# Kernel tuning notes

Measured on AMD Instinct MI355X. Metric: run time of the kernel, lower is better.

Reference implementation:

```python
import jax, jax.numpy as jnp
import numpy as np

EPS = 1e-5

def activation_quant(x):
    # per-token absmax int8 quant-dequant (BitNet b1.58)
    scale = 127.0 / jnp.clip(jnp.max(jnp.abs(x), axis=-1, keepdims=True), EPS)
    q = jnp.clip(jnp.round(x * scale), -128.0, 127.0) / scale
    return q

def weight_quant(w):
    # per-tensor ternary quant-dequant: scale by 1/mean|w|, round, clamp to {-1,0,1}
    scale = 1.0 / jnp.clip(jnp.mean(jnp.abs(w)), EPS)
    q = jnp.clip(jnp.round(w * scale), -1.0, 1.0) / scale
    return q

def bitlinear(x, w):
    # x: [b, s, in], w: [out, in] (nn.Linear layout)
    return jnp.einsum('bsi,oi->bso', activation_quant(x), weight_quant(w))

def setup_inputs() -> dict:
    key = jax.random.key(0)
    k1, k2, k3, k4 = jax.random.split(key, 4)
    B, S, H, I = 2, 2048, 4096, 11008
    x = jax.random.normal(k1, (B, S, H), dtype=jnp.float32)
    w_gate = jax.random.normal(k2, (I, H), dtype=jnp.float32) * (1.0 / np.sqrt(H))
    w_up = jax.random.normal(k3, (I, H), dtype=jnp.float32) * (1.0 / np.sqrt(H))
    w_down = jax.random.normal(k4, (H, I), dtype=jnp.float32) * (1.0 / np.sqrt(I))
    return {"x": x, "w_gate": w_gate, "w_up": w_up, "w_down": w_down}

def reference(x, w_gate, w_up, w_down):
    g = bitlinear(x, w_gate)           # [B, S, I]
    u = bitlinear(x, w_up)             # [B, S, I]
    h = jnp.square(jax.nn.relu(g)) * u  # ReLU^2 gating
    return bitlinear(h, w_down)        # [B, S, H]
```

## Files before the change

kernel.cpp:

```cpp
#include <hip/hip_runtime.h>
#include <stdint.h>

#define TOKENS 4096
#define HDIM   4096
#define IDIM   11008
#define WELEMS 45088768L

using i32x4 = __attribute__((ext_vector_type(4))) int;
using s8x16 = __attribute__((ext_vector_type(16))) signed char;

__device__ __forceinline__ void async_load16(const void* g, void* l) {
  __builtin_amdgcn_global_load_lds(
      (const __attribute__((address_space(1))) void*)g,
      (__attribute__((address_space(3))) void*)l, 16, 0, 0);
}

__global__ __launch_bounds__(256) void wsum_kernel(
    const float* __restrict__ w0, const float* __restrict__ w1,
    const float* __restrict__ w2, double* __restrict__ dsum) {
  const float* w = (blockIdx.y == 0) ? w0 : (blockIdx.y == 1) ? w1 : w2;
  const long n4 = WELEMS / 4;
  long i = (long)blockIdx.x * blockDim.x + threadIdx.x;
  const long stride = (long)gridDim.x * blockDim.x;
  double s = 0.0;
  for (; i < n4; i += stride) {
    float4 v = ((const float4*)w)[i];
    s += (double)fabsf(v.x); s += (double)fabsf(v.y);
    s += (double)fabsf(v.z); s += (double)fabsf(v.w);
  }
  __shared__ double red[256];
  red[threadIdx.x] = s;
  __syncthreads();
  for (int off = 128; off; off >>= 1) {
    if (threadIdx.x < (unsigned)off) red[threadIdx.x] += red[threadIdx.x + off];
    __syncthreads();
  }
  if (threadIdx.x == 0) atomicAdd(&dsum[blockIdx.y], red[0]);
}

__global__ void wscale_kernel(const double* __restrict__ dsum, double* __restrict__ wsc) {
  int i = threadIdx.x;
  if (i < 3) {
    double mean = dsum[i] / (double)WELEMS;
    wsc[i] = 1.0 / fmax(mean, 1e-5);
  }
}

__global__ __launch_bounds__(256) void wquant_kernel(
    const float* __restrict__ w0, const float* __restrict__ w1, const float* __restrict__ w2,
    int8_t* __restrict__ q0, int8_t* __restrict__ q1, int8_t* __restrict__ q2,
    const double* __restrict__ wsc) {
  const int wi = blockIdx.y;
  const float* w = (wi == 0) ? w0 : (wi == 1) ? w1 : w2;
  int8_t* q = (wi == 0) ? q0 : (wi == 1) ? q1 : q2;
  const double sc = wsc[wi];
  long c = (long)blockIdx.x * blockDim.x + threadIdx.x;
  if (c * 16 >= WELEMS) return;
  const float4* src = (const float4*)(w + c * 16);
  s8x16 outv;
  #pragma unroll
  for (int j = 0; j < 4; ++j) {
    float4 v = src[j];
    double t0 = rint((double)v.x * sc); t0 = fmin(fmax(t0, -1.0), 1.0);
    double t1 = rint((double)v.y * sc); t1 = fmin(fmax(t1, -1.0), 1.0);
    double t2 = rint((double)v.z * sc); t2 = fmin(fmax(t2, -1.0), 1.0);
    double t3 = rint((double)v.w * sc); t3 = fmin(fmax(t3, -1.0), 1.0);
    outv[j*4+0] = (signed char)(int)t0; outv[j*4+1] = (signed char)(int)t1;
    outv[j*4+2] = (signed char)(int)t2; outv[j*4+3] = (signed char)(int)t3;
  }
  *(s8x16*)(q + c * 16) = outv;
}

__global__ __launch_bounds__(256) void xquant_kernel(
    const float* __restrict__ x, int8_t* __restrict__ xq, double* __restrict__ sx) {
  const int row = blockIdx.x;
  const float* xr = x + (long)row * HDIM;
  const float4* xr4 = (const float4*)xr;
  float m = 0.f;
  for (int i = threadIdx.x; i < HDIM / 4; i += 256) {
    float4 v = xr4[i];
    m = fmaxf(m, fmaxf(fmaxf(fabsf(v.x), fabsf(v.y)), fmaxf(fabsf(v.z), fabsf(v.w))));
  }
  __shared__ float red[256];
  red[threadIdx.x] = m;
  __syncthreads();
  for (int off = 128; off; off >>= 1) {
    if (threadIdx.x < (unsigned)off) red[threadIdx.x] = fmaxf(red[threadIdx.x], red[threadIdx.x + off]);
    __syncthreads();
  }
  __shared__ double s_sc;
  if (threadIdx.x == 0) {
    double sc = 127.0 / fmax((double)red[0], 1e-5);
    sx[row] = sc;
    s_sc = sc;
  }
  __syncthreads();
  const double sc = s_sc;
  s8x16 outv;
  #pragma unroll
  for (int j = 0; j < 4; ++j) {
    float4 v = xr4[threadIdx.x * 4 + j];
    double t0 = rint((double)v.x * sc); t0 = fmin(fmax(t0, -128.0), 127.0);
    double t1 = rint((double)v.y * sc); t1 = fmin(fmax(t1, -128.0), 127.0);
    double t2 = rint((double)v.z * sc); t2 = fmin(fmax(t2, -128.0), 127.0);
    double t3 = rint((double)v.w * sc); t3 = fmin(fmax(t3, -128.0), 127.0);
    outv[j*4+0] = (signed char)(int)t0; outv[j*4+1] = (signed char)(int)t1;
    outv[j*4+2] = (signed char)(int)t2; outv[j*4+3] = (signed char)(int)t3;
  }
  *(s8x16*)(xq + (long)row * HDIM + threadIdx.x * 16) = outv;
}

__global__ __launch_bounds__(256, 2) void gemm1_kernel(
    const int8_t* __restrict__ Aq, const int8_t* __restrict__ Bg, const int8_t* __restrict__ Bu,
    const double* __restrict__ sx, const double* __restrict__ wsc,
    float* __restrict__ H, unsigned int* __restrict__ hmax) {
  __shared__ __align__(16) int8_t As[128 * 64];
  __shared__ __align__(16) int8_t Bsg[128 * 64];
  __shared__ __align__(16) int8_t Bsu[128 * 64];
  __shared__ unsigned int smax[128];

  const int tid = threadIdx.x;
  const int l = tid & 63;
  const int wv = tid >> 6;
  const int wm = (wv >> 1) * 64;
  const int wn = (wv & 1) * 64;
  const int row0 = blockIdx.y * 128;
  const int col0 = blockIdx.x * 128;

  i32x4 accg[4][4], accu[4][4];
  #pragma unroll
  for (int i = 0; i < 4; i++)
    #pragma unroll
    for (int j = 0; j < 4; j++) { accg[i][j] = i32x4{0,0,0,0}; accu[i][j] = i32x4{0,0,0,0}; }

  const int off0 = tid * 16;
  const int rs = off0 >> 6;
  const int cs = off0 & 63;

  for (int k0 = 0; k0 < HDIM; k0 += 64) {
    #pragma unroll
    for (int s = 0; s < 2; ++s) {
      const int off = off0 + s * 4096;
      const int r = rs + s * 64;
      const long ga = (long)(row0 + r) * HDIM + k0 + cs;
      const long gb = (long)(col0 + r) * HDIM + k0 + cs;
      async_load16(Aq + ga, As + off);
      async_load16(Bg + gb, Bsg + off);
      async_load16(Bu + gb, Bsu + off);
    }
    __syncthreads();
    const int kq = (l >> 4) * 16;
    const int mr = l & 15;
    i32x4 af[4], bgf[4], buf_[4];
    #pragma unroll
    for (int t = 0; t < 4; t++) af[t] = *(const i32x4*)(As + (wm + t * 16 + mr) * 64 + kq);
    #pragma unroll
    for (int t = 0; t < 4; t++) {
      bgf[t] = *(const i32x4*)(Bsg + (wn + t * 16 + mr) * 64 + kq);
      buf_[t] = *(const i32x4*)(Bsu + (wn + t * 16 + mr) * 64 + kq);
    }
    #pragma unroll
    for (int mt = 0; mt < 4; mt++)
      #pragma unroll
      for (int nt = 0; nt < 4; nt++) {
        accg[mt][nt] = __builtin_amdgcn_mfma_i32_16x16x64_i8(af[mt], bgf[nt], accg[mt][nt], 0, 0, 0);
        accu[mt][nt] = __builtin_amdgcn_mfma_i32_16x16x64_i8(af[mt], buf_[nt], accu[mt][nt], 0, 0, 0);
      }
    __syncthreads();
  }

  if (tid < 128) smax[tid] = 0u;
  __syncthreads();
  const double swg = wsc[0], swu = wsc[1];
  #pragma unroll
  for (int mt = 0; mt < 4; mt++) {
    #pragma unroll
    for (int r = 0; r < 4; r++) {
      const int grow = wm + mt * 16 + (l >> 4) * 4 + r;
      const long growg = row0 + grow;
      const double sxr = sx[growg];
      const double dg = 1.0 / (sxr * swg);
      const double du = 1.0 / (sxr * swu);
      float am = 0.f;
      #pragma unroll
      for (int nt = 0; nt < 4; nt++) {
        const float g = (float)((double)accg[mt][nt][r] * dg);
        const float u = (float)((double)accu[mt][nt][r] * du);
        const float gr = g > 0.f ? g * g : 0.f;
        const float h = gr * u;
        H[growg * IDIM + col0 + wn + nt * 16 + (l & 15)] = h;
        am = fmaxf(am, fabsf(h));
      }
      atomicMax(&smax[grow], __float_as_uint(am));
    }
  }
  __syncthreads();
  if (tid < 128) atomicMax(&hmax[row0 + tid], smax[tid]);
}

__global__ __launch_bounds__(256) void hquant_kernel(
    const float* __restrict__ H, int8_t* __restrict__ hq, const unsigned int* __restrict__ hmax) {
  const long c = (long)blockIdx.x * blockDim.x + threadIdx.x;
  const long nchunks = (long)TOKENS * IDIM / 16;
  if (c >= nchunks) return;
  const int row = (int)(c / (IDIM / 16));
  const double sc = 127.0 / fmax((double)__uint_as_float(hmax[row]), 1e-5);
  const float4* src = (const float4*)(H + c * 16);
  s8x16 outv;
  #pragma unroll
  for (int j = 0; j < 4; ++j) {
    float4 v = src[j];
    double t0 = rint((double)v.x * sc); t0 = fmin(fmax(t0, -128.0), 127.0);
    double t1 = rint((double)v.y * sc); t1 = fmin(fmax(t1, -128.0), 127.0);
    double t2 = rint((double)v.z * sc); t2 = fmin(fmax(t2, -128.0), 127.0);
    double t3 = rint((double)v.w * sc); t3 = fmin(fmax(t3, -128.0), 127.0);
    outv[j*4+0] = (signed char)(int)t0; outv[j*4+1] = (signed char)(int)t1;
    outv[j*4+2] = (signed char)(int)t2; outv[j*4+3] = (signed char)(int)t3;
  }
  *(s8x16*)(hq + c * 16) = outv;
}

__global__ __launch_bounds__(256, 2) void gemm2_kernel(
    const int8_t* __restrict__ Aq, const int8_t* __restrict__ Bq,
    const unsigned int* __restrict__ hmax, const double* __restrict__ wsc,
    float* __restrict__ out) {
  __shared__ __align__(16) int8_t As[128 * 64];
  __shared__ __align__(16) int8_t Bs[128 * 64];

  const int tid = threadIdx.x;
  const int l = tid & 63;
  const int wv = tid >> 6;
  const int wm = (wv >> 1) * 64;
  const int wn = (wv & 1) * 64;
  const int row0 = blockIdx.y * 128;
  const int col0 = blockIdx.x * 128;

  i32x4 acc[4][4];
  #pragma unroll
  for (int i = 0; i < 4; i++)
    #pragma unroll
    for (int j = 0; j < 4; j++) acc[i][j] = i32x4{0,0,0,0};

  const int off0 = tid * 16;
  const int rs = off0 >> 6;
  const int cs = off0 & 63;

  for (int k0 = 0; k0 < IDIM; k0 += 64) {
    #pragma unroll
    for (int s = 0; s < 2; ++s) {
      const int off = off0 + s * 4096;
      const int r = rs + s * 64;
      const long ga = (long)(row0 + r) * IDIM + k0 + cs;
      const long gb = (long)(col0 + r) * IDIM + k0 + cs;
      async_load16(Aq + ga, As + off);
      async_load16(Bq + gb, Bs + off);
    }
    __syncthreads();
    const int kq = (l >> 4) * 16;
    const int mr = l & 15;
    i32x4 af[4], bf[4];
    #pragma unroll
    for (int t = 0; t < 4; t++) af[t] = *(const i32x4*)(As + (wm + t * 16 + mr) * 64 + kq);
    #pragma unroll
    for (int t = 0; t < 4; t++) bf[t] = *(const i32x4*)(Bs + (wn + t * 16 + mr) * 64 + kq);
    #pragma unroll
    for (int mt = 0; mt < 4; mt++)
      #pragma unroll
      for (int nt = 0; nt < 4; nt++)
        acc[mt][nt] = __builtin_amdgcn_mfma_i32_16x16x64_i8(af[mt], bf[nt], acc[mt][nt], 0, 0, 0);
    __syncthreads();
  }

  const double swd = wsc[2];
  #pragma unroll
  for (int mt = 0; mt < 4; mt++) {
    #pragma unroll
    for (int r = 0; r < 4; r++) {
      const int grow = wm + mt * 16 + (l >> 4) * 4 + r;
      const long growg = row0 + grow;
      const double shr = 127.0 / fmax((double)__uint_as_float(hmax[growg]), 1e-5);
      const double inv = 1.0 / (shr * swd);
      #pragma unroll
      for (int nt = 0; nt < 4; nt++)
        out[growg * HDIM + col0 + wn + nt * 16 + (l & 15)] = (float)((double)acc[mt][nt][r] * inv);
    }
  }
}

extern "C" void kernel_launch(void* const* d_in, const int* in_sizes, int n_in,
                              void* d_out, int out_size, void* d_ws, size_t ws_size,
                              hipStream_t stream) {
  const float* x  = (const float*)d_in[0];
  const float* wg = (const float*)d_in[1];
  const float* wu = (const float*)d_in[2];
  const float* wd = (const float*)d_in[3];
  float* out = (float*)d_out;

  char* ws = (char*)d_ws;
  double*   dsum  = (double*)ws;
  double*   wsc   = (double*)(ws + 32);
  double*   sx    = (double*)(ws + 64);
  unsigned* hmaxb = (unsigned*)(ws + 64 + TOKENS * 8);
  int8_t*   xq    = (int8_t*)(ws + 131072);
  int8_t*   wqg   = xq + (long)TOKENS * HDIM;
  int8_t*   wqu   = wqg + WELEMS;
  int8_t*   wqd   = wqu + WELEMS;
  int8_t*   hq    = wqd + WELEMS;
  float*    H     = (float*)(hq + WELEMS);
  const size_t needed = 131072 + (size_t)TOKENS * HDIM + 4 * (size_t)WELEMS
                      + (size_t)TOKENS * IDIM * sizeof(float);
  if (ws_size < needed) {
    hipMemsetAsync(d_out, 0, (size_t)out_size * sizeof(float), stream);
    return;
  }

  hipMemsetAsync(ws, 0, 65536, stream);

  { dim3 g(1024, 3); wsum_kernel<<<g, 256, 0, stream>>>(wg, wu, wd, dsum); }
  wscale_kernel<<<1, 64, 0, stream>>>(dsum, wsc);
  { dim3 g((unsigned)(WELEMS / (256 * 16)), 3);
    wquant_kernel<<<g, 256, 0, stream>>>(wg, wu, wd, wqg, wqu, wqd, wsc); }
  xquant_kernel<<<TOKENS, 256, 0, stream>>>(x, xq, sx);
  { dim3 g(IDIM / 128, TOKENS / 128);
    gemm1_kernel<<<g, 256, 0, stream>>>(xq, wqg, wqu, sx, wsc, H, hmaxb); }
  hquant_kernel<<<(unsigned)((long)TOKENS * IDIM / 16 / 256), 256, 0, stream>>>(H, hq, hmaxb);
  { dim3 g(HDIM / 128, TOKENS / 128);
    gemm2_kernel<<<g, 256, 0, stream>>>(hq, wqd, hmaxb, wsc, out); }
}
```

Baseline: 1.385 ms.

## Rewrite int8 GEMMs with 256-row tiles, double-buffered LDS, swizzle and phased pipeline

Both int8 GEMM kernels move to 512-thread blocks with larger tiles (256x128 for gemm1, 256x256 for gemm2) and a K-step of 128. Global-to-LDS async loads are double-buffered and interleaved with MFMA phases, using partial vmcnt waits, barriers and setprio. LDS addresses are XOR-swizzled to avoid bank conflicts. The aim is to hide memory latency behind MFMA work and raise data reuse, in exchange for much larger LDS use and more register pressure, which can lower occupancy.

```diff
diff --git a/kernel.cpp b/kernel.cpp
--- a/kernel.cpp
+++ b/kernel.cpp
@@ -14,6 +14,30 @@
       (const __attribute__((address_space(1))) void*)g,
       (__attribute__((address_space(3))) void*)l, 16, 0, 0);
 }
+
+__device__ __forceinline__ void stage128(
+    const int8_t* __restrict__ g, long grow0, long ld, long kbase,
+    int8_t* lds, int tid) {
+  #pragma unroll
+  for (int j = 0; j < 2; ++j) {
+    const int idx  = j * 512 + tid;
+    const int row  = idx >> 3;
+    const int slot = idx & 7;
+    const int8_t* src = g + (grow0 + row) * ld + kbase + ((slot ^ (row & 7)) << 4);
+    async_load16(src, lds + idx * 16);
+  }
+}
+
+#define PH_SYNC() \
+  asm volatile("s_waitcnt vmcnt(4)" ::: "memory"); \
+  __builtin_amdgcn_s_barrier(); \
+  asm volatile("s_waitcnt lgkmcnt(0)" ::: "memory"); \
+  __builtin_amdgcn_sched_barrier(0); \
+  __builtin_amdgcn_s_setprio(1)
+
+#define PH_END() \
+  __builtin_amdgcn_s_setprio(0); \
+  __builtin_amdgcn_s_barrier()
 
 __global__ __launch_bounds__(256) void wsum_kernel(
     const float* __restrict__ w0, const float* __restrict__ w1,
@@ -110,92 +134,150 @@
   *(s8x16*)(xq + (long)row * HDIM + threadIdx.x * 16) = outv;
 }
 
-__global__ __launch_bounds__(256, 2) void gemm1_kernel(
+
+__device__ __forceinline__ void g1_rdA(const int8_t* buf, int mh, int abase0,
+                                       int kq, int swl, i32x4 afr[2][2]) {
+  #pragma unroll
+  for (int m = 0; m < 2; ++m)
+    #pragma unroll
+    for (int ks = 0; ks < 2; ++ks)
+      afr[m][ks] = *(const i32x4*)(buf + abase0 + m * 2048 + mh * 16384 +
+                                   ((((ks << 2) | kq) ^ swl) << 4));
+}
+
+__device__ __forceinline__ void g1_rdB(const int8_t* buf, int bbase0,
+                                       int kq, int swl, i32x4 bfr[4][2]) {
+  #pragma unroll
+  for (int n = 0; n < 4; ++n)
+    #pragma unroll
+    for (int ks = 0; ks < 2; ++ks)
+      bfr[n][ks] = *(const i32x4*)(buf + bbase0 + n * 2048 +
+                                   ((((ks << 2) | kq) ^ swl) << 4));
+}
+
+__device__ __forceinline__ void g1_mfma(i32x4 acc[4][4], const i32x4 afr[2][2],
+                                        const i32x4 bfr[4][2], int mh) {
+  #pragma unroll
+  for (int ks = 0; ks < 2; ++ks)
+    #pragma unroll
+    for (int m = 0; m < 2; ++m)
+      #pragma unroll
+      for (int n = 0; n < 4; ++n)
+        acc[mh*2+m][n] = __builtin_amdgcn_mfma_i32_16x16x64_i8(
+            afr[m][ks], bfr[n][ks], acc[mh*2+m][n], 0, 0, 0);
+}
+
+__global__ __launch_bounds__(512, 2) void gemm1_kernel(
     const int8_t* __restrict__ Aq, const int8_t* __restrict__ Bg, const int8_t* __restrict__ Bu,
     const double* __restrict__ sx, const double* __restrict__ wsc,
     float* __restrict__ H, unsigned int* __restrict__ hmax) {
-  __shared__ __align__(16) int8_t As[128 * 64];
-  __shared__ __align__(16) int8_t Bsg[128 * 64];
-  __shared__ __align__(16) int8_t Bsu[128 * 64];
-  __shared__ unsigned int smax[128];
+  __shared__ __align__(16) int8_t As[2][256 * 128];
+  __shared__ __align__(16) int8_t Bgs[2][128 * 128];
+  __shared__ __align__(16) int8_t Bus[2][128 * 128];
+  __shared__ unsigned int smax[256];
 
   const int tid = threadIdx.x;
-  const int l = tid & 63;
-  const int wv = tid >> 6;
-  const int wm = (wv >> 1) * 64;
-  const int wn = (wv & 1) * 64;
-  const int row0 = blockIdx.y * 128;
+  const int l   = tid & 63;
+  const int wid = tid >> 6;
+  const int wr  = wid >> 1;
+  const int wc  = wid & 1;
+  const int mr  = l & 15;
+  const int kq  = l >> 4;
+  const int swl = l & 7;
+  const int row0 = blockIdx.y * 256;
   const int col0 = blockIdx.x * 128;
 
+  const int abase0 = (wr * 32 + mr) * 128;
+  const int bbase0 = (wc * 64 + mr) * 128;
+
+  if (tid < 256) smax[tid] = 0u;
+
+  stage128(Aq, row0,        HDIM, 0, As[0],          tid);
+  stage128(Bg, col0,        HDIM, 0, Bgs[0],         tid);
+  stage128(Bu, col0,        HDIM, 0, Bus[0],         tid);
+  stage128(Aq, row0 + 128,  HDIM, 0, As[0] + 16384,  tid);
+  asm volatile("s_waitcnt vmcnt(4)" ::: "memory");
+  __builtin_amdgcn_s_barrier();
+
   i32x4 accg[4][4], accu[4][4];
   #pragma unroll
-  for (int i = 0; i < 4; i++)
-    #pragma unroll
-    for (int j = 0; j < 4; j++) { accg[i][j] = i32x4{0,0,0,0}; accu[i][j] = i32x4{0,0,0,0}; }
-
-  const int off0 = tid * 16;
-  const int rs = off0 >> 6;
-  const int cs = off0 & 63;
-
-  for (int k0 = 0; k0 < HDIM; k0 += 64) {
-    #pragma unroll
-    for (int s = 0; s < 2; ++s) {
-      const int off = off0 + s * 4096;
-      const int r = rs + s * 64;
-      const long ga = (long)(row0 + r) * HDIM + k0 + cs;
-      const long gb = (long)(col0 + r) * HDIM + k0 + cs;
-      async_load16(Aq + ga, As + off);
-      async_load16(Bg + gb, Bsg + off);
-      async_load16(Bu + gb, Bsu + off);
-    }
-    __syncthreads();
-    const int kq = (l >> 4) * 16;
-    const int mr = l & 15;
-    i32x4 af[4], bgf[4], buf_[4];
-    #pragma unroll
-    for (int t = 0; t < 4; t++) af[t] = *(const i32x4*)(As + (wm + t * 16 + mr) * 64 + kq);
-    #pragma unroll
-    for (int t = 0; t < 4; t++) {
-      bgf[t] = *(const i32x4*)(Bsg + (wn + t * 16 + mr) * 64 + kq);
-      buf_[t] = *(const i32x4*)(Bsu + (wn + t * 16 + mr) * 64 + kq);
-    }
-    #pragma unroll
-    for (int mt = 0; mt < 4; mt++)
-      #pragma unroll
-      for (int nt = 0; nt < 4; nt++) {
-        accg[mt][nt] = __builtin_amdgcn_mfma_i32_16x16x64_i8(af[mt], bgf[nt], accg[mt][nt], 0, 0, 0);
-        accu[mt][nt] = __builtin_amdgcn_mfma_i32_16x16x64_i8(af[mt], buf_[nt], accu[mt][nt], 0, 0, 0);
-      }
-    __syncthreads();
-  }
-
-  if (tid < 128) smax[tid] = 0u;
-  __syncthreads();
+  for (int i = 0; i < 4; ++i)
+    #pragma unroll
+    for (int j = 0; j < 4; ++j) { accg[i][j] = (i32x4){0,0,0,0}; accu[i][j] = (i32x4){0,0,0,0}; }
+  i32x4 afr[2][2], bgf[4][2], buv[4][2];
+
+  #pragma unroll 1
+  for (int I = 0; I < 16; ++I) {
+    const long k1 = (long)(2 * I + 1) * 128;
+    const long k2 = (2 * I + 2 < 32) ? (long)(2 * I + 2) * 128 : 0;
+
+    g1_rdA(As[0], 0, abase0, kq, swl, afr);
+    g1_rdB(Bgs[0], bbase0, kq, swl, bgf);
+    stage128(Aq, row0, HDIM, k1, As[1], tid);
+    PH_SYNC();
+    g1_mfma(accg, afr, bgf, 0);
+    PH_END();
+    g1_rdB(Bus[0], bbase0, kq, swl, buv);
+    stage128(Bg, col0, HDIM, k1, Bgs[1], tid);
+    PH_SYNC();
+    g1_mfma(accu, afr, buv, 0);
+    PH_END();
+    g1_rdA(As[0], 1, abase0, kq, swl, afr);
+    stage128(Bu, col0, HDIM, k1, Bus[1], tid);
+    PH_SYNC();
+    g1_mfma(accg, afr, bgf, 1);
+    PH_END();
+    stage128(Aq, row0 + 128, HDIM, k1, As[1] + 16384, tid);
+    PH_SYNC();
+    g1_mfma(accu, afr, buv, 1);
+    PH_END();
+    g1_rdA(As[1], 0, abase0, kq, swl, afr);
+    g1_rdB(Bgs[1], bbase0, kq, swl, bgf);
+    stage128(Aq, row0, HDIM, k2, As[0], tid);
+    PH_SYNC();
+    g1_mfma(accg, afr, bgf, 0);
+    PH_END();
+    g1_rdB(Bus[1], bbase0, kq, swl, buv);
+    stage128(Bg, col0, HDIM, k2, Bgs[0], tid);
+    PH_SYNC();
+    g1_mfma(accu, afr, buv, 0);
+    PH_END();
+    g1_rdA(As[1], 1, abase0, kq, swl, afr);
+    stage128(Bu, col0, HDIM, k2, Bus[0], tid);
+    PH_SYNC();
+    g1_mfma(accg, afr, bgf, 1);
+    PH_END();
+    stage128(Aq, row0 + 128, HDIM, k2, As[0] + 16384, tid);
+    PH_SYNC();
+    g1_mfma(accu, afr, buv, 1);
+    PH_END();
+  }
+
   const double swg = wsc[0], swu = wsc[1];
   #pragma unroll
-  for (int mt = 0; mt < 4; mt++) {
-    #pragma unroll
-    for (int r = 0; r < 4; r++) {
-      const int grow = wm + mt * 16 + (l >> 4) * 4 + r;
-      const long growg = row0 + grow;
-      const double sxr = sx[growg];
+  for (int t = 0; t < 4; ++t) {
+    #pragma unroll
+    for (int r = 0; r < 4; ++r) {
+      const int lrow = (t >> 1) * 128 + wr * 32 + (t & 1) * 16 + kq * 4 + r;
+      const long grow = row0 + lrow;
+      const double sxr = sx[grow];
       const double dg = 1.0 / (sxr * swg);
       const double du = 1.0 / (sxr * swu);
       float am = 0.f;
       #pragma unroll
-      for (int nt = 0; nt < 4; nt++) {
-        const float g = (float)((double)accg[mt][nt][r] * dg);
-        const float u = (float)((double)accu[mt][nt][r] * du);
+      for (int n = 0; n < 4; ++n) {
+        const float g = (float)((double)accg[t][n][r] * dg);
+        const float u = (float)((double)accu[t][n][r] * du);
         const float gr = g > 0.f ? g * g : 0.f;
         const float h = gr * u;
-        H[growg * IDIM + col0 + wn + nt * 16 + (l & 15)] = h;
+        H[grow * IDIM + col0 + wc * 64 + n * 16 + mr] = h;
         am = fmaxf(am, fabsf(h));
       }
-      atomicMax(&smax[grow], __float_as_uint(am));
+      atomicMax(&smax[lrow], __float_as_uint(am));
     }
   }
   __syncthreads();
-  if (tid < 128) atomicMax(&hmax[row0 + tid], smax[tid]);
+  if (tid < 256) atomicMax(&hmax[row0 + tid], smax[tid]);
 }
 
 __global__ __launch_bounds__(256) void hquant_kernel(
@@ -220,69 +302,134 @@
   *(s8x16*)(hq + c * 16) = outv;
 }
 
-__global__ __launch_bounds__(256, 2) void gemm2_kernel(
+
+__device__ __forceinline__ void g2_rdA(const int8_t* buf, int mh, int abase0,
+                                       int kq, int swl, i32x4 afr[4][2]) {
+  #pragma unroll
+  for (int m = 0; m < 4; ++m)
+    #pragma unroll
+    for (int ks = 0; ks < 2; ++ks)
+      afr[m][ks] = *(const i32x4*)(buf + abase0 + m * 2048 + mh * 16384 +
+                                   ((((ks << 2) | kq) ^ swl) << 4));
+}
+
+__device__ __forceinline__ void g2_rdB(const int8_t* buf, int nh, int bbase0,
+                                       int kq, int swl, i32x4 bfr[4][2]) {
+  #pragma unroll
+  for (int n = 0; n < 2; ++n)
+    #pragma unroll
+    for (int ks = 0; ks < 2; ++ks)
+      bfr[nh*2+n][ks] = *(const i32x4*)(buf + bbase0 + n * 2048 + nh * 16384 +
+                                        ((((ks << 2) | kq) ^ swl) << 4));
+}
+
+__device__ __forceinline__ void g2_mfma(i32x4 acc[8][4], const i32x4 afr[4][2],
+                                        const i32x4 bfr[4][2], int mh, int nh) {
+  #pragma unroll
+  for (int ks = 0; ks < 2; ++ks)
+    #pragma unroll
+    for (int m = 0; m < 4; ++m)
+      #pragma unroll
+      for (int n = 0; n < 2; ++n)
+        acc[mh*4+m][nh*2+n] = __builtin_amdgcn_mfma_i32_16x16x64_i8(
+            afr[m][ks], bfr[nh*2+n][ks], acc[mh*4+m][nh*2+n], 0, 0, 0);
+}
+
+__global__ __launch_bounds__(512, 2) void gemm2_kernel(
     const int8_t* __restrict__ Aq, const int8_t* __restrict__ Bq,
     const unsigned int* __restrict__ hmax, const double* __restrict__ wsc,
     float* __restrict__ out) {
-  __shared__ __align__(16) int8_t As[128 * 64];
-  __shared__ __align__(16) int8_t Bs[128 * 64];
+  __shared__ __align__(16) int8_t As[2][256 * 128];
+  __shared__ __align__(16) int8_t Bs[2][256 * 128];
 
   const int tid = threadIdx.x;
-  const int l = tid & 63;
-  const int wv = tid >> 6;
-  const int wm = (wv >> 1) * 64;
-  const int wn = (wv & 1) * 64;
-  const int row0 = blockIdx.y * 128;
-  const int col0 = blockIdx.x * 128;
-
-  i32x4 acc[4][4];
-  #pragma unroll
-  for (int i = 0; i < 4; i++)
-    #pragma unroll
-    for (int j = 0; j < 4; j++) acc[i][j] = i32x4{0,0,0,0};
-
-  const int off0 = tid * 16;
-  const int rs = off0 >> 6;
-  const int cs = off0 & 63;
-
-  for (int k0 = 0; k0 < IDIM; k0 += 64) {
-    #pragma unroll
-    for (int s = 0; s < 2; ++s) {
-      const int off = off0 + s * 4096;
-      const int r = rs + s * 64;
-      const long ga = (long)(row0 + r) * IDIM + k0 + cs;
-      const long gb = (long)(col0 + r) * IDIM + k0 + cs;
-      async_load16(Aq + ga, As + off);
-      async_load16(Bq + gb, Bs + off);
-    }
-    __syncthreads();
-    const int kq = (l >> 4) * 16;
-    const int mr = l & 15;
-    i32x4 af[4], bf[4];
-    #pragma unroll
-    for (int t = 0; t < 4; t++) af[t] = *(const i32x4*)(As + (wm + t * 16 + mr) * 64 + kq);
-    #pragma unroll
-    for (int t = 0; t < 4; t++) bf[t] = *(const i32x4*)(Bs + (wn + t * 16 + mr) * 64 + kq);
-    #pragma unroll
-    for (int mt = 0; mt < 4; mt++)
-      #pragma unroll
-      for (int nt = 0; nt < 4; nt++)
-        acc[mt][nt] = __builtin_amdgcn_mfma_i32_16x16x64_i8(af[mt], bf[nt], acc[mt][nt], 0, 0, 0);
-    __syncthreads();
+  const int l   = tid & 63;
+  const int wid = tid >> 6;
+  const int wr  = wid >> 2;
+  const int wc  = wid & 3;
+  const int mr  = l & 15;
+  const int kq  = l >> 4;
+  const int swl = l & 7;
+  const int row0 = blockIdx.y * 256;
+  const int col0 = blockIdx.x * 256;
+
+  const int abase0 = (wr * 64 + mr) * 128;
+  const int bbase0 = (wc * 32 + mr) * 128;
+
+  stage128(Aq, row0,        IDIM, 0, As[0],          tid);
+  stage128(Bq, col0,        IDIM, 0, Bs[0],          tid);
+  stage128(Bq, col0 + 128,  IDIM, 0, Bs[0] + 16384,  tid);
+  stage128(Aq, row0 + 128,  IDIM, 0, As[0] + 16384,  tid);
+  asm volatile("s_waitcnt vmcnt(4)" ::: "memory");
+  __builtin_amdgcn_s_barrier();
+
+  i32x4 acc[8][4];
+  #pragma unroll
+  for (int i = 0; i < 8; ++i)
+    #pragma unroll
+    for (int j = 0; j < 4; ++j) acc[i][j] = (i32x4){0,0,0,0};
+  i32x4 afr[4][2], bfr[4][2];
+
+  #pragma unroll 1
+  for (int I = 0; I < 43; ++I) {
+    const long k1 = (long)(2 * I + 1) * 128;
+    const long k2 = (2 * I + 2 < 86) ? (long)(2 * I + 2) * 128 : 0;
+
+    g2_rdA(As[0], 0, abase0, kq, swl, afr);
+    g2_rdB(Bs[0], 0, bbase0, kq, swl, bfr);
+    stage128(Aq, row0, IDIM, k1, As[1], tid);
+    PH_SYNC();
+    g2_mfma(acc, afr, bfr, 0, 0);
+    PH_END();
+    g2_rdB(Bs[0], 1, bbase0, kq, swl, bfr);
+    stage128(Bq, col0, IDIM, k1, Bs[1], tid);
+    PH_SYNC();
+    g2_mfma(acc, afr, bfr, 0, 1);
+    PH_END();
+    g2_rdA(As[0], 1, abase0, kq, swl, afr);
+    stage128(Bq, col0 + 128, IDIM, k1, Bs[1] + 16384, tid);
+    PH_SYNC();
+    g2_mfma(acc, afr, bfr, 1, 0);
+    PH_END();
+    stage128(Aq, row0 + 128, IDIM, k1, As[1] + 16384, tid);
+    PH_SYNC();
+    g2_mfma(acc, afr, bfr, 1, 1);
+    PH_END();
+    g2_rdA(As[1], 0, abase0, kq, swl, afr);
+    g2_rdB(Bs[1], 0, bbase0, kq, swl, bfr);
+    stage128(Aq, row0, IDIM, k2, As[0], tid);
+    PH_SYNC();
+    g2_mfma(acc, afr, bfr, 0, 0);
+    PH_END();
+    g2_rdB(Bs[1], 1, bbase0, kq, swl, bfr);
+    stage128(Bq, col0, IDIM, k2, Bs[0], tid);
+    PH_SYNC();
+    g2_mfma(acc, afr, bfr, 0, 1);
+    PH_END();
+    g2_rdA(As[1], 1, abase0, kq, swl, afr);
+    stage128(Bq, col0 + 128, IDIM, k2, Bs[0] + 16384, tid);
+    PH_SYNC();
+    g2_mfma(acc, afr, bfr, 1, 0);
+    PH_END();
+    stage128(Aq, row0 + 128, IDIM, k2, As[0] + 16384, tid);
+    PH_SYNC();
+    g2_mfma(acc, afr, bfr, 1, 1);
+    PH_END();
   }
 
   const double swd = wsc[2];
   #pragma unroll
-  for (int mt = 0; mt < 4; mt++) {
-    #pragma unroll
-    for (int r = 0; r < 4; r++) {
-      const int grow = wm + mt * 16 + (l >> 4) * 4 + r;
-      const long growg = row0 + grow;
-      const double shr = 127.0 / fmax((double)__uint_as_float(hmax[growg]), 1e-5);
+  for (int t = 0; t < 8; ++t) {
+    #pragma unroll
+    for (int r = 0; r < 4; ++r) {
+      const int lrow = (t >> 2) * 128 + wr * 64 + (t & 3) * 16 + kq * 4 + r;
+      const long grow = row0 + lrow;
+      const double shr = 127.0 / fmax((double)__uint_as_float(hmax[grow]), 1e-5);
       const double inv = 1.0 / (shr * swd);
       #pragma unroll
-      for (int nt = 0; nt < 4; nt++)
-        out[growg * HDIM + col0 + wn + nt * 16 + (l & 15)] = (float)((double)acc[mt][nt][r] * inv);
+      for (int n = 0; n < 4; ++n)
+        out[grow * HDIM + col0 + (n >> 1) * 128 + wc * 32 + (n & 1) * 16 + mr] =
+            (float)((double)acc[t][n][r] * inv);
     }
   }
 }
@@ -321,9 +468,9 @@
   { dim3 g((unsigned)(WELEMS / (256 * 16)), 3);
     wquant_kernel<<<g, 256, 0, stream>>>(wg, wu, wd, wqg, wqu, wqd, wsc); }
   xquant_kernel<<<TOKENS, 256, 0, stream>>>(x, xq, sx);
-  { dim3 g(IDIM / 128, TOKENS / 128);
-    gemm1_kernel<<<g, 256, 0, stream>>>(xq, wqg, wqu, sx, wsc, H, hmaxb); }
+  { dim3 g(IDIM / 128, TOKENS / 256);
+    gemm1_kernel<<<g, 512, 0, stream>>>(xq, wqg, wqu, sx, wsc, H, hmaxb); }
   hquant_kernel<<<(unsigned)((long)TOKENS * IDIM / 16 / 256), 256, 0, stream>>>(H, hq, hmaxb);
-  { dim3 g(HDIM / 128, TOKENS / 128);
-    gemm2_kernel<<<g, 256, 0, stream>>>(hq, wqd, hmaxb, wsc, out); }
-}
+  { dim3 g(HDIM / 256, TOKENS / 256);
+    gemm2_kernel<<<g, 512, 0, stream>>>(hq, wqd, hmaxb, wsc, out); }
+}
```

Result: faster. 1.215 ms (-12.2%).
